# Optimization experiments

Measured on AMD Instinct MI355X. Metric: run time of the kernel, lower is better.

The kernel has to match this reference:

```python
import jax, jax.numpy as jnp
import numpy as np

B, T, C = 32, 512, 32
D, H, DFF, NL = 512, 8, 2048, 3
P, STRIDE, PAD = 16, 8, 8
N = (T - P) // STRIDE + 2  # 64 patches
E = D // H


def _sinusoidal_pe(n, d):
    pos = np.arange(n, dtype=np.float32)[:, None]
    div = np.exp(np.arange(0, d, 2, dtype=np.float32) * -(np.log(10000.0) / d))
    pe = np.zeros((n, d), np.float32)
    pe[:, 0::2] = np.sin(pos * div)
    pe[:, 1::2] = np.cos(pos * div)
    return jnp.asarray(pe)


def setup_inputs() -> dict:
    key = jax.random.key(0)
    ks = jax.random.split(key, 16)
    s = 0.02
    inp = {
        'x_enc': jax.random.normal(ks[0], (B, T, C), jnp.float32),
        'W_val': jax.random.normal(ks[1], (P, D), jnp.float32) * s,
        'Wq': jax.random.normal(ks[2], (NL, D, D), jnp.float32) * s,
        'bq': jnp.zeros((NL, D), jnp.float32),
        'Wk': jax.random.normal(ks[3], (NL, D, D), jnp.float32) * s,
        'bk': jnp.zeros((NL, D), jnp.float32),
        'Wv': jax.random.normal(ks[4], (NL, D, D), jnp.float32) * s,
        'bv': jnp.zeros((NL, D), jnp.float32),
        'Wo': jax.random.normal(ks[5], (NL, D, D), jnp.float32) * s,
        'bo': jnp.zeros((NL, D), jnp.float32),
        'Wc1': jax.random.normal(ks[6], (NL, D, DFF), jnp.float32) * s,
        'bc1': jnp.zeros((NL, DFF), jnp.float32),
        'Wc2': jax.random.normal(ks[7], (NL, DFF, D), jnp.float32) * s,
        'bc2': jnp.zeros((NL, D), jnp.float32),
        'ln1_g': jnp.ones((NL, D), jnp.float32),
        'ln1_b': jnp.zeros((NL, D), jnp.float32),
        'ln2_g': jnp.ones((NL, D), jnp.float32),
        'ln2_b': jnp.zeros((NL, D), jnp.float32),
        'bn_g': jnp.ones((D,), jnp.float32),
        'bn_b': jnp.zeros((D,), jnp.float32),
        'W_head': jax.random.normal(ks[8], (D * N, T), jnp.float32) * s,
        'b_head': jnp.zeros((T,), jnp.float32),
    }
    return inp


def _ln(x, g, b, eps=1e-5):
    m = x.mean(-1, keepdims=True)
    v = ((x - m) ** 2).mean(-1, keepdims=True)
    return (x - m) / jnp.sqrt(v + eps) * g + b


def reference(x_enc, W_val, Wq, bq, Wk, bk, Wv, bv, Wo, bo, Wc1, bc1, Wc2, bc2,
              ln1_g, ln1_b, ln2_g, ln2_b, bn_g, bn_b, W_head, b_head):
    pe = _sinusoidal_pe(N, D)
    # instance normalization over time (means detached, as in torch .detach())
    means = jax.lax.stop_gradient(x_enc.mean(axis=1, keepdims=True))
    x = x_enc - means
    stdev = jnp.sqrt(x.var(axis=1, keepdims=True) + 1e-5)  # [B,1,C]
    x = x / stdev
    x = x.transpose(0, 2, 1)  # [B, C, T]
    # replication pad right by PAD, then unfold into patches [B,C,N,P]
    x = jnp.concatenate([x, jnp.broadcast_to(x[..., -1:], x.shape[:-1] + (PAD,))], axis=-1)
    idx = jnp.arange(N)[:, None] * STRIDE + jnp.arange(P)[None, :]
    xp = x[..., idx]
    tok = xp.reshape(B * C, N, P) @ W_val + pe  # [B*C, N, D]

    scale = 1.0 / np.sqrt(E).astype(np.float32)
    for i in range(NL):
        q = (tok @ Wq[i] + bq[i]).reshape(-1, N, H, E)
        k = (tok @ Wk[i] + bk[i]).reshape(-1, N, H, E)
        v = (tok @ Wv[i] + bv[i]).reshape(-1, N, H, E)
        scores = jnp.einsum('blhe,bshe->bhls', q, k)
        A = jax.nn.softmax(scale * scores, axis=-1)
        V = jnp.einsum('bhls,bshd->blhd', A, v).reshape(-1, N, D)
        tok = tok + (V @ Wo[i] + bo[i])
        y = _ln(tok, ln1_g[i], ln1_b[i])
        y = jax.nn.gelu(y @ Wc1[i] + bc1[i], approximate=False) @ Wc2[i] + bc2[i]
        tok = _ln(tok + y, ln2_g[i], ln2_b[i])

    # BatchNorm1d over d_model channels (batch statistics, biased variance)
    m = tok.mean(axis=(0, 1))
    var = tok.var(axis=(0, 1))
    tok = (tok - m) / jnp.sqrt(var + 1e-5) * bn_g + bn_b

    enc = tok.reshape(B, C, N, D).transpose(0, 1, 3, 2).reshape(B, C, D * N)
    dec = enc @ W_head + b_head          # [B, C, T]
    dec = dec.transpose(0, 2, 1)          # [B, T, C]
    dec = dec * stdev[:, 0, :][:, None, :] + means[:, 0, :][:, None, :]
    return dec
```

## Files before the change

kernel.cpp:

```cpp
#include <hip/hip_runtime.h>
#include <math.h>

namespace {
constexpr int kB = 32, kT = 512, kC = 32, kD = 512, kDFF = 2048, kNL = 3;
constexpr int kP = 16, kStride = 8, kN = 64;
constexpr int kR = kB * kC;
constexpr int kM = kR * kN;
constexpr size_t kWbElems = (size_t)1536 * 512 + 512 * 512 + 2048 * 512 + 512 * 2048;
}

typedef unsigned short u16;
typedef __attribute__((ext_vector_type(8))) short short8;
typedef __attribute__((ext_vector_type(4))) float f32x4;

__device__ __forceinline__ float b2f(u16 u) {
    return __uint_as_float(((unsigned int)u) << 16);
}
__device__ __forceinline__ u16 f2b(float f) {
    unsigned int x = __float_as_uint(f);
    return (u16)((x + 0x7fffu + ((x >> 16) & 1u)) >> 16);
}

__device__ __forceinline__ void async_copy16(const u16* g, u16* l) {
    __builtin_amdgcn_global_load_lds(
        (const __attribute__((address_space(1))) unsigned int*)g,
        (__attribute__((address_space(3))) unsigned int*)l, 16, 0, 0);
}

__global__ void fill_kernel(float* __restrict__ p, float val, int n)
{
    int i = blockIdx.x * blockDim.x + threadIdx.x;
    if (i < n) p[i] = val;
}

__global__ __launch_bounds__(256) void instnorm_stats_kernel(
    const float* __restrict__ x, float* __restrict__ means, float* __restrict__ stdev)
{
    int b = blockIdx.x;
    int c = threadIdx.x & 31;
    int g = threadIdx.x >> 5;
    float s = 0.f, sq = 0.f;
    for (int t = g; t < kT; t += 8) {
        float v = x[(size_t)(b * kT + t) * kC + c];
        s += v; sq += v * v;
    }
    __shared__ float ss[8][32], ssq[8][32];
    ss[g][c] = s; ssq[g][c] = sq;
    __syncthreads();
    if (g == 0) {
        float S = 0.f, SQ = 0.f;
        for (int i = 0; i < 8; i++) { S += ss[i][c]; SQ += ssq[i][c]; }
        float m = S / kT;
        float var = SQ / kT - m * m;
        means[b * kC + c] = m;
        stdev[b * kC + c] = sqrtf(var + 1e-5f);
    }
}

__global__ __launch_bounds__(256) void pe_kernel(float* __restrict__ pe)
{
    int i = blockIdx.x * 256 + threadIdx.x;
    int n = i >> 9, d = i & 511;
    int j = d >> 1;
    float freq = expf(-(float)(2 * j) * (9.210340371976184f / (float)kD));
    float ang = (float)n * freq;
    pe[i] = (d & 1) ? cosf(ang) : sinf(ang);
}

__global__ __launch_bounds__(256) void patch_embed_kernel(
    const float* __restrict__ x, const float* __restrict__ Wval,
    const float* __restrict__ means, const float* __restrict__ stdev,
    const float* __restrict__ pe, u16* __restrict__ tok)
{
    __shared__ float xn[kT + 16];
    __shared__ float wv[kP * kD];
    const int r = blockIdx.x;
    const int b = r >> 5, c = r & 31;
    const int tid = threadIdx.x;
    const float mean = means[r], inv = 1.f / stdev[r];
    for (int t = tid; t < kT; t += 256)
        xn[t] = (x[(size_t)(b * kT + t) * kC + c] - mean) * inv;
    if (tid < 16)
        xn[kT + tid] = (x[(size_t)(b * kT + kT - 1) * kC + c] - mean) * inv;
    for (int i = tid * 4; i < kP * kD; i += 1024)
        *(float4*)&wv[i] = *(const float4*)&Wval[i];
    __syncthreads();

    const int lane = tid & 63, w = tid >> 6;
    const int d0 = lane << 3;
    for (int g = 0; g < 16; g++) {
        const int n = g * 4 + w;
        const float* pen = pe + (size_t)n * kD + d0;
        float acc[8];
        #pragma unroll
        for (int j = 0; j < 8; j++) acc[j] = pen[j];
        #pragma unroll
        for (int p = 0; p < kP; p++) {
            float xv = xn[n * kStride + p];
            const float* wp = &wv[p * kD + d0];
            #pragma unroll
            for (int j = 0; j < 8; j++) acc[j] += xv * wp[j];
        }
        short8 o;
        #pragma unroll
        for (int j = 0; j < 8; j++) o[j] = (short)f2b(acc[j]);
        *(short8*)&tok[((size_t)r * 64 + n) * kD + d0] = o;
    }
}

__global__ __launch_bounds__(256) void transpose_cvt_kernel(
    const float* __restrict__ in, u16* __restrict__ outp,
    const float* __restrict__ scale,
    int ldi, int ldo, int zin, int zout)
{
    __shared__ float tile[64][65];
    const float* ib = in + (size_t)blockIdx.z * zin;
    u16* ob = outp + (size_t)blockIdx.z * zout;
    int k0 = blockIdx.x * 64, n0 = blockIdx.y * 64;
    int tn = threadIdx.x & 63, tk0 = threadIdx.x >> 6;
    #pragma unroll
    for (int kk = tk0; kk < 64; kk += 4) {
        float sc = scale ? scale[k0 + kk] : 1.f;
        tile[kk][tn] = ib[(size_t)(k0 + kk) * ldi + n0 + tn] * sc;
    }
    __syncthreads();
    int wk = threadIdx.x & 63, wn0 = threadIdx.x >> 6;
    #pragma unroll
    for (int nn = wn0; nn < 64; nn += 4)
        ob[(size_t)(n0 + nn) * ldo + k0 + wk] = f2b(tile[wk][nn]);
}

__global__ __launch_bounds__(256) void transpose_cvt4_kernel(
    const float* __restrict__ in0, const float* __restrict__ in1,
    const float* __restrict__ in2, const float* __restrict__ in3,
    u16* __restrict__ outQKV, u16* __restrict__ outO)
{
    __shared__ float tile[64][65];
    int z = blockIdx.z;
    const float* ib = (z == 0) ? in0 : (z == 1) ? in1 : (z == 2) ? in2 : in3;
    u16* ob = (z < 3) ? outQKV + (size_t)z * 512 * 512 : outO;
    int k0 = blockIdx.x * 64, n0 = blockIdx.y * 64;
    int tn = threadIdx.x & 63, tk0 = threadIdx.x >> 6;
    #pragma unroll
    for (int kk = tk0; kk < 64; kk += 4)
        tile[kk][tn] = ib[(size_t)(k0 + kk) * 512 + n0 + tn];
    __syncthreads();
    int wk = threadIdx.x & 63, wn0 = threadIdx.x >> 6;
    #pragma unroll
    for (int nn = wn0; nn < 64; nn += 4)
        ob[(size_t)(n0 + nn) * 512 + k0 + wk] = f2b(tile[wk][nn]);
}

template<int EPI>
__device__ __forceinline__ void gemm_body(
    const u16* __restrict__ A, const u16* __restrict__ B,
    const float* __restrict__ bias, const float* __restrict__ auxb1,
    const float* __restrict__ auxb2,
    u16* __restrict__ C0, u16* __restrict__ C1, u16* __restrict__ C2,
    float* __restrict__ fout,
    int K, int lda, int ldb, int ldc)
{
    __shared__ alignas(16) u16 As[128 * 64];
    __shared__ alignas(16) u16 Bs[128 * 64];

    const int tid  = threadIdx.x;
    const int lane = tid & 63;
    const int wave = tid >> 6;
    const int wm   = wave >> 1;
    const int wn   = wave & 1;

    const int nwg  = gridDim.x * gridDim.y;
    const int orig = blockIdx.y * gridDim.x + blockIdx.x;
    const int qq = nwg >> 3, rr = nwg & 7;
    const int xcd = orig & 7, loc = orig >> 3;
    const int wg  = (xcd < rr) ? (xcd * (qq + 1) + loc)
                               : (rr * (qq + 1) + (xcd - rr) * qq + loc);
    const int row0 = (wg / gridDim.x) * 128;
    const int col0 = (wg % gridDim.x) * 128;
    const size_t zoff = (size_t)blockIdx.z * K;

    const int srow = tid >> 3;
    const int scol = (((tid & 7) ^ (srow & 7)) << 3);
    const u16* const Ag = A + (size_t)(row0 + srow) * lda + zoff + scol;
    const u16* const Bg = B + (size_t)(col0 + srow) * ldb + zoff + scol;
    u16* const AsW = As + (wave << 9);
    u16* const BsW = Bs + (wave << 9);

    const int fr = lane & 15;
    const int pc = (lane >> 4) ^ (lane & 7);
    const int a0 = ((wm << 6) + fr) * 64 + (pc << 3);
    const int a1 = ((wm << 6) + fr) * 64 + ((pc ^ 4) << 3);
    const int b0 = ((wn << 6) + fr) * 64 + (pc << 3);
    const int b1 = ((wn << 6) + fr) * 64 + ((pc ^ 4) << 3);

    short8 af[4], bfr[4];
    f32x4 acc[4][4];
    #pragma unroll
    for (int i = 0; i < 4; i++)
        #pragma unroll
        for (int j = 0; j < 4; j++)
            acc[i][j] = (f32x4){0.f, 0.f, 0.f, 0.f};

    for (int kb = 0; kb < K; kb += 64) {
        __syncthreads();
        #pragma unroll
        for (int c = 0; c < 4; c++) {
            async_copy16(Ag + kb + (size_t)(c * 32) * lda, AsW + c * 2048);
            async_copy16(Bg + kb + (size_t)(c * 32) * ldb, BsW + c * 2048);
        }
        __syncthreads();
        #pragma unroll
        for (int mi = 0; mi < 4; mi++) af[mi]  = *(const short8*)&As[a0 + (mi << 10)];
        #pragma unroll
        for (int ni = 0; ni < 4; ni++) bfr[ni] = *(const short8*)&Bs[b0 + (ni << 10)];
        #pragma unroll
        for (int mi = 0; mi < 4; mi++)
            #pragma unroll
            for (int ni = 0; ni < 4; ni++)
                acc[mi][ni] = __builtin_amdgcn_mfma_f32_16x16x32_bf16(
                    af[mi], bfr[ni], acc[mi][ni], 0, 0, 0);
        #pragma unroll
        for (int mi = 0; mi < 4; mi++) af[mi]  = *(const short8*)&As[a1 + (mi << 10)];
        #pragma unroll
        for (int ni = 0; ni < 4; ni++) bfr[ni] = *(const short8*)&Bs[b1 + (ni << 10)];
        #pragma unroll
        for (int mi = 0; mi < 4; mi++)
            #pragma unroll
            for (int ni = 0; ni < 4; ni++)
                acc[mi][ni] = __builtin_amdgcn_mfma_f32_16x16x32_bf16(
                    af[mi], bfr[ni], acc[mi][ni], 0, 0, 0);
    }

    const int er = (lane >> 4) << 2;
    const int ec = lane & 15;
    u16* dsel = C0;
    const float* bsel = bias;
    if (EPI == 0) {
        int sub = col0 >> 9;
        dsel = (sub == 0) ? C0 : ((sub == 1) ? C1 : C2);
        bsel = (sub == 0) ? bias : ((sub == 1) ? auxb1 : auxb2);
    }
    #pragma unroll
    for (int mi = 0; mi < 4; mi++) {
        #pragma unroll
        for (int ni = 0; ni < 4; ni++) {
            #pragma unroll
            for (int i = 0; i < 4; i++) {
                int r  = row0 + (wm << 6) + (mi << 4) + er + i;
                int cc = col0 + (wn << 6) + (ni << 4) + ec;
                float v = acc[mi][ni][i];
                if (EPI == 0) {
                    int cl = cc & 511;
                    dsel[(size_t)r * 512 + cl] = f2b(v + bsel[cl]);
                } else if (EPI == 1) {
                    size_t o = (size_t)r * ldc + cc;
                    float bb2 = bias ? bias[cc] : 0.f;
                    C0[o] = f2b(b2f(C0[o]) + v + bb2);
                } else if (EPI == 2) {
                    size_t o = (size_t)r * ldc + cc;
                    float z = v + bias[cc];
                    C0[o] = f2b(0.5f * z * (1.f + erff(z * 0.7071067811865475f)));
                } else {
                    fout[((size_t)blockIdx.z << 19) + (size_t)r * ldc + cc] = v;
                }
            }
        }
    }
}

#define GEMM_ARGS \
    const u16* __restrict__ A, const u16* __restrict__ B, \
    const float* __restrict__ bias, const float* __restrict__ auxb1, \
    const float* __restrict__ auxb2, \
    u16* __restrict__ C0, u16* __restrict__ C1, u16* __restrict__ C2, \
    float* __restrict__ fout, \
    int K, int lda, int ldb, int ldc
#define GEMM_PASS A, B, bias, auxb1, auxb2, C0, C1, C2, fout, K, lda, ldb, ldc

__global__ __launch_bounds__(256) void gemm_qkv(GEMM_ARGS)   { gemm_body<0>(GEMM_PASS); }
__global__ __launch_bounds__(256) void gemm_resid(GEMM_ARGS) { gemm_body<1>(GEMM_PASS); }
__global__ __launch_bounds__(256) void gemm_gelu(GEMM_ARGS)  { gemm_body<2>(GEMM_PASS); }
__global__ __launch_bounds__(256) void gemm_head(GEMM_ARGS)  { gemm_body<3>(GEMM_PASS); }

__global__ __launch_bounds__(256) void vtr_kernel(u16* __restrict__ v)
{
    __shared__ u16 tl[4][64 * 72];
    const int tid = threadIdx.x;
    const int wave = tid >> 6, lane = tid & 63;
    const int sr = lane >> 3, ch = lane & 7;
    const int tile = blockIdx.x * 4 + wave;
    const int series = tile >> 3, h = tile & 7;
    u16* g = v + (size_t)series * 64 * kD + h * 64;
    u16* T = tl[wave];
    short8 rd[8];
    #pragma unroll
    for (int r = 0; r < 8; r++)
        rd[r] = *(const short8*)(g + (size_t)(r * 8 + sr) * kD + ch * 8);
    #pragma unroll
    for (int r = 0; r < 8; r++)
        *(short8*)&T[(r * 8 + sr) * 72 + ch * 8] = rd[r];
    __syncthreads();
    #pragma unroll
    for (int r = 0; r < 8; r++) {
        short8 wr;
        #pragma unroll
        for (int q = 0; q < 8; q++)
            wr[q] = (short)T[(ch * 8 + q) * 72 + (r * 8 + sr)];
        *(short8*)(g + (size_t)(r * 8 + sr) * kD + ch * 8) = wr;
    }
}

__global__ __launch_bounds__(256) void attn_mfma_kernel(
    u16* __restrict__ qbuf, const u16* __restrict__ kbuf,
    const u16* __restrict__ vbuf)
{
    __shared__ u16 P[4][64 * 64];
    const int tid = threadIdx.x;
    const int wave = tid >> 6, lane = tid & 63;
    const int quad = lane >> 4, l15 = lane & 15;
    const size_t base = (size_t)blockIdx.x * 64 * kD;
    u16* Pw = P[wave];

    for (int hh = 0; hh < 2; hh++) {
        const int h = wave * 2 + hh;
        const u16* qh = qbuf + base + h * 64;
        const u16* kh = kbuf + base + h * 64;
        const u16* vh = vbuf + base + h * 64;

        short8 af[4][2], bf[4][2];
        #pragma unroll
        for (int mi = 0; mi < 4; mi++)
            #pragma unroll
            for (int kt = 0; kt < 2; kt++)
                af[mi][kt] = *(const short8*)(qh + (size_t)(mi * 16 + l15) * kD
                                              + kt * 32 + quad * 8);
        #pragma unroll
        for (int ni = 0; ni < 4; ni++)
            #pragma unroll
            for (int kt = 0; kt < 2; kt++)
                bf[ni][kt] = *(const short8*)(kh + (size_t)(ni * 16 + l15) * kD
                                              + kt * 32 + quad * 8);
        f32x4 S[4][4];
        #pragma unroll
        for (int mi = 0; mi < 4; mi++)
            #pragma unroll
            for (int ni = 0; ni < 4; ni++)
                S[mi][ni] = (f32x4){0.f, 0.f, 0.f, 0.f};
        #pragma unroll
        for (int mi = 0; mi < 4; mi++)
            #pragma unroll
            for (int ni = 0; ni < 4; ni++) {
                S[mi][ni] = __builtin_amdgcn_mfma_f32_16x16x32_bf16(
                    af[mi][0], bf[ni][0], S[mi][ni], 0, 0, 0);
                S[mi][ni] = __builtin_amdgcn_mfma_f32_16x16x32_bf16(
                    af[mi][1], bf[ni][1], S[mi][ni], 0, 0, 0);
            }

        #pragma unroll
        for (int mi = 0; mi < 4; mi++) {
            #pragma unroll
            for (int i = 0; i < 4; i++) {
                float mx = -1e30f;
                #pragma unroll
                for (int ni = 0; ni < 4; ni++) {
                    float v = S[mi][ni][i] * 0.125f;
                    S[mi][ni][i] = v;
                    mx = fmaxf(mx, v);
                }
                #pragma unroll
                for (int off = 1; off < 16; off <<= 1)
                    mx = fmaxf(mx, __shfl_xor(mx, off));
                float sum = 0.f;
                #pragma unroll
                for (int ni = 0; ni < 4; ni++) {
                    float e = expf(S[mi][ni][i] - mx);
                    S[mi][ni][i] = e;
                    sum += e;
                }
                #pragma unroll
                for (int off = 1; off < 16; off <<= 1)
                    sum += __shfl_xor(sum, off);
                float inv = 1.f / sum;
                #pragma unroll
                for (int ni = 0; ni < 4; ni++)
                    Pw[(mi * 16 + quad * 4 + i) * 64 + ni * 16 + l15] =
                        f2b(S[mi][ni][i] * inv);
            }
        }
        __syncthreads();

        short8 bv[4][2];
        #pragma unroll
        for (int ni = 0; ni < 4; ni++)
            #pragma unroll
            for (int kt = 0; kt < 2; kt++)
                bv[ni][kt] = *(const short8*)(vh + (size_t)(ni * 16 + l15) * kD
                                              + kt * 32 + quad * 8);
        short8 pa[4][2];
        #pragma unroll
        for (int mi = 0; mi < 4; mi++)
            #pragma unroll
            for (int kt = 0; kt < 2; kt++)
                pa[mi][kt] = *(const short8*)&Pw[(mi * 16 + l15) * 64
                                                 + kt * 32 + quad * 8];
        f32x4 O[4][4];
        #pragma unroll
        for (int mi = 0; mi < 4; mi++)
            #pragma unroll
            for (int ni = 0; ni < 4; ni++)
                O[mi][ni] = (f32x4){0.f, 0.f, 0.f, 0.f};
        #pragma unroll
        for (int mi = 0; mi < 4; mi++)
            #pragma unroll
            for (int ni = 0; ni < 4; ni++) {
                O[mi][ni] = __builtin_amdgcn_mfma_f32_16x16x32_bf16(
                    pa[mi][0], bv[ni][0], O[mi][ni], 0, 0, 0);
                O[mi][ni] = __builtin_amdgcn_mfma_f32_16x16x32_bf16(
                    pa[mi][1], bv[ni][1], O[mi][ni], 0, 0, 0);
            }
        u16* qo = qbuf + base + h * 64;
        #pragma unroll
        for (int mi = 0; mi < 4; mi++)
            #pragma unroll
            for (int ni = 0; ni < 4; ni++)
                #pragma unroll
                for (int i = 0; i < 4; i++)
                    qo[(size_t)(mi * 16 + quad * 4 + i) * kD + ni * 16 + l15] =
                        f2b(O[mi][ni][i]);
        __syncthreads();
    }
}

__global__ __launch_bounds__(256) void ln_kernel(
    const u16* __restrict__ x, const float* __restrict__ g,
    const float* __restrict__ bb, u16* __restrict__ y)
{
    size_t row = (size_t)blockIdx.x * 4 + (threadIdx.x >> 6);
    int lane = threadIdx.x & 63;
    int d0 = lane << 3;
    short8 xv = *(const short8*)&x[row * kD + d0];
    float v[8];
    float s = 0.f;
    #pragma unroll
    for (int i = 0; i < 8; i++) {
        v[i] = b2f((u16)xv[i]);
        s += v[i];
    }
    #pragma unroll
    for (int off = 32; off; off >>= 1) s += __shfl_xor(s, off);
    float mean = s * (1.f / kD);
    float sq = 0.f;
    #pragma unroll
    for (int i = 0; i < 8; i++) { float d = v[i] - mean; sq += d * d; }
    #pragma unroll
    for (int off = 32; off; off >>= 1) sq += __shfl_xor(sq, off);
    float inv = 1.f / sqrtf(sq * (1.f / kD) + 1e-5f);
    short8 o;
    #pragma unroll
    for (int i = 0; i < 8; i++)
        o[i] = (short)f2b((v[i] - mean) * inv * g[d0 + i] + bb[d0 + i]);
    *(short8*)&y[row * kD + d0] = o;
}

__global__ void zero_kernel(float* __restrict__ p, int n)
{
    int i = blockIdx.x * blockDim.x + threadIdx.x;
    if (i < n) p[i] = 0.f;
}

__global__ __launch_bounds__(512) void bn_stats_kernel(
    const u16* __restrict__ tok, float* __restrict__ sums, float* __restrict__ sumsq)
{
    int d = threadIdx.x;
    float s = 0.f, sq = 0.f;
    int row0 = blockIdx.x * 256;
    for (int row = row0; row < row0 + 256; row++) {
        float v = b2f(tok[(size_t)row * kD + d]);
        s += v; sq += v * v;
    }
    atomicAdd(&sums[d], s);
    atomicAdd(&sumsq[d], sq);
}

__global__ __launch_bounds__(512) void bn_final_kernel(
    const float* __restrict__ sums, const float* __restrict__ sumsq,
    const float* __restrict__ g, const float* __restrict__ bb,
    float* __restrict__ scale, float* __restrict__ shift)
{
    int d = threadIdx.x;
    float mean = sums[d] / (float)kM;
    float var = sumsq[d] / (float)kM - mean * mean;
    float sc = g[d] / sqrtf(var + 1e-5f);
    scale[d] = sc;
    shift[d] = bb[d] - mean * sc;
}

__global__ __launch_bounds__(512) void head_shift_kernel(
    const float* __restrict__ W_head, const float* __restrict__ shift,
    float* __restrict__ shiftW)
{
    int t = threadIdx.x;
    int r0 = blockIdx.x * 512;
    float s = 0.f;
    for (int r = r0; r < r0 + 512; r++)
        s += shift[r >> 6] * W_head[(size_t)r * 512 + t];
    atomicAdd(&shiftW[t], s);
}

__global__ __launch_bounds__(256) void head_reduce_kernel(
    const float* __restrict__ part, const float* __restrict__ b_head,
    const float* __restrict__ shiftW,
    const float* __restrict__ stdev, const float* __restrict__ means,
    float* __restrict__ out)
{
    int j = blockIdx.x * 256 + threadIdx.x;
    int r = j >> 9, t = j & 511;
    float s = 0.f;
    #pragma unroll
    for (int z = 0; z < 16; z++) s += part[((size_t)z << 19) + j];
    int b = r >> 5, c = r & 31;
    out[(((size_t)b * kT + t) << 5) + c] =
        (s + shiftW[t] + b_head[t]) * stdev[r] + means[r];
}

extern "C" void kernel_launch(void* const* d_in, const int* in_sizes, int n_in,
                              void* d_out, int out_size, void* d_ws, size_t ws_size,
                              hipStream_t stream)
{
    const float* x_enc  = (const float*)d_in[0];
    const float* W_val  = (const float*)d_in[1];
    const float* Wq     = (const float*)d_in[2];
    const float* bq     = (const float*)d_in[3];
    const float* Wk     = (const float*)d_in[4];
    const float* bk     = (const float*)d_in[5];
    const float* Wv     = (const float*)d_in[6];
    const float* bv     = (const float*)d_in[7];
    const float* Wo     = (const float*)d_in[8];
    const float* bo     = (const float*)d_in[9];
    const float* Wc1    = (const float*)d_in[10];
    const float* bc1    = (const float*)d_in[11];
    const float* Wc2    = (const float*)d_in[12];
    const float* bc2    = (const float*)d_in[13];
    const float* ln1_g  = (const float*)d_in[14];
    const float* ln1_b  = (const float*)d_in[15];
    const float* ln2_g  = (const float*)d_in[16];
    const float* ln2_b  = (const float*)d_in[17];
    const float* bn_g   = (const float*)d_in[18];
    const float* bn_b   = (const float*)d_in[19];
    const float* W_head = (const float*)d_in[20];
    const float* b_head = (const float*)d_in[21];
    float* out = (float*)d_out;

    const size_t tailBytes = (2 * kR + 5 * kD + 64 * kD) * sizeof(float);
    const size_t headWb = (size_t)512 * 32768;
    int CH = 0; size_t unit = 0, region = 0;
    const int cands[4] = {1024, 512, 256, 128};
    for (int ci = 0; ci < 4; ci++) {
        size_t u = (size_t)cands[ci] * 64 * kD;
        size_t reg = 3 * u + kWbElems;
        if (reg < headWb) reg = headWb;
        size_t need = ((size_t)kM * kD + reg) * 2 + tailBytes;
        if (need <= ws_size) { CH = cands[ci]; unit = u; region = reg; break; }
    }
    if (CH == 0) {
        hipLaunchKernelGGL(fill_kernel, dim3((out_size + 255) / 256), dim3(256), 0,
                           stream, out, 1.0e6f, out_size);
        return;
    }
    const int nch = kR / CH;
    const int chRows = CH * 64;

    u16* tokb = (u16*)d_ws;
    u16* s0  = tokb + (size_t)kM * kD;
    u16* s1  = s0 + unit;
    u16* s2  = s1 + unit;
    u16* wbL = s2 + unit;
    u16* wbH = s0;
    u16* wQKV = wbL;
    u16* wO   = wQKV + (size_t)1536 * 512;
    u16* wC1  = wO + (size_t)512 * 512;
    u16* wC2  = wC1 + (size_t)2048 * 512;
    float* tail = (float*)(s0 + region);
    float* means    = tail;
    float* stdevp   = means + kR;
    float* bn_sums  = stdevp + kR;
    float* bn_sumsq = bn_sums + kD;
    float* shiftW   = bn_sumsq + kD;
    float* bn_scale = shiftW + kD;
    float* bn_shift = bn_scale + kD;
    float* peT      = bn_shift + kD;

    hipLaunchKernelGGL(pe_kernel, dim3(128), dim3(256), 0, stream, peT);
    hipLaunchKernelGGL(instnorm_stats_kernel, dim3(kB), dim3(256), 0, stream,
                       x_enc, means, stdevp);
    hipLaunchKernelGGL(patch_embed_kernel, dim3(kR), dim3(256), 0, stream,
                       x_enc, W_val, means, stdevp, peT, tokb);

    const dim3 blk(256);
    const int mt = chRows / 128;

    for (int i = 0; i < kNL; i++) {
        const float* Wq_i = Wq + (size_t)i * kD * kD;
        const float* Wk_i = Wk + (size_t)i * kD * kD;
        const float* Wv_i = Wv + (size_t)i * kD * kD;
        const float* Wo_i = Wo + (size_t)i * kD * kD;
        const float* Wc1_i = Wc1 + (size_t)i * kD * kDFF;
        const float* Wc2_i = Wc2 + (size_t)i * kDFF * kD;
        const float* bq_i = bq + i * kD, *bk_i = bk + i * kD, *bv_i = bv + i * kD;

        hipLaunchKernelGGL(transpose_cvt4_kernel, dim3(8, 8, 4), blk, 0, stream,
                           Wq_i, Wk_i, Wv_i, Wo_i, wQKV, wO);
        hipLaunchKernelGGL(transpose_cvt_kernel, dim3(8, 32, 1), blk, 0, stream,
                           Wc1_i, wC1, nullptr, kDFF, kD, 0, 0);
        hipLaunchKernelGGL(transpose_cvt_kernel, dim3(32, 8, 1), blk, 0, stream,
                           Wc2_i, wC2, nullptr, kD, kDFF, 0, 0);

        for (int ch = 0; ch < nch; ch++) {
            u16* tokc = tokb + (size_t)ch * chRows * kD;
            hipLaunchKernelGGL(gemm_qkv, dim3(12, mt, 1), blk, 0, stream,
                               tokc, wQKV, bq_i, bk_i, bv_i, s0, s1, s2,
                               nullptr, kD, kD, kD, kD);
            hipLaunchKernelGGL(vtr_kernel, dim3(CH * 2), blk, 0, stream, s2);
            hipLaunchKernelGGL(attn_mfma_kernel, dim3(CH), blk, 0, stream,
                               s0, s1, s2);
            hipLaunchKernelGGL(gemm_resid, dim3(4, mt, 1), blk, 0, stream,
                               s0, wO, bo + i * kD, nullptr, nullptr,
                               tokc, nullptr, nullptr, nullptr,
                               kD, kD, kD, kD);
            hipLaunchKernelGGL(ln_kernel, dim3(chRows / 4), blk, 0, stream,
                               tokc, ln1_g + i * kD, ln1_b + i * kD, s0);
            for (int half = 0; half < 2; half++) {
                const u16* wc1h = wC1 + (size_t)half * 1024 * 512;
                const u16* wc2h = wC2 + (size_t)half * 1024;
                const float* bc1h = bc1 + (size_t)i * kDFF + half * 1024;
                hipLaunchKernelGGL(gemm_gelu, dim3(8, mt, 1), blk, 0, stream,
                                   s0, wc1h, bc1h, nullptr, nullptr,
                                   s1, nullptr, nullptr, nullptr,
                                   kD, kD, kD, 1024);
                hipLaunchKernelGGL(gemm_resid, dim3(4, mt, 1), blk, 0, stream,
                                   s1, wc2h, (half == 0) ? (bc2 + i * kD) : nullptr,
                                   nullptr, nullptr, tokc, nullptr, nullptr,
                                   nullptr, 1024, 1024, kDFF, kD);
            }
            hipLaunchKernelGGL(ln_kernel, dim3(chRows / 4), blk, 0, stream,
                               tokc, ln2_g + i * kD, ln2_b + i * kD, tokc);
        }
    }

    hipLaunchKernelGGL(zero_kernel, dim3(6), dim3(256), 0, stream, bn_sums, 3 * kD);
    hipLaunchKernelGGL(bn_stats_kernel, dim3(kM / 256), dim3(512), 0, stream,
                       tokb, bn_sums, bn_sumsq);
    hipLaunchKernelGGL(bn_final_kernel, dim3(1), dim3(512), 0, stream,
                       bn_sums, bn_sumsq, bn_g, bn_b, bn_scale, bn_shift);
    hipLaunchKernelGGL(head_shift_kernel, dim3(64), dim3(512), 0, stream,
                       W_head, bn_shift, shiftW);

    hipLaunchKernelGGL(transpose_cvt_kernel, dim3(8, 8, 64), blk, 0, stream,
                       W_head, wbH, bn_scale, 64 * 512, 32768, 512, 512);
    hipLaunchKernelGGL(gemm_head, dim3(4, 8, 16), blk, 0, stream,
                       tokb, wbH, nullptr, nullptr, nullptr,
                       nullptr, nullptr, nullptr, (float*)s1,
                       2048, 32768, 32768, kT);
    hipLaunchKernelGGL(head_reduce_kernel, dim3(kR * kT / 256), blk, 0, stream,
                       (const float*)s1, b_head, shiftW, stdevp, means, out);
}
```

Measured before the change: 3.186 ms.

## Compute V transposed directly via swapped GEMM, drop separate V transpose kernel

The V projection is split out of the fused QKV GEMM and computed as W_v·tok^T with a new row-bias epilogue, so V lands already transposed (head-dim major, token contiguous). This removes the vtr_kernel pass and its global read/write, and the attention kernel now reads V with a configurable stride. The head_shift kernel is also reworked to use 512 blocks with one shift scalar per block, which adds parallelism. The transposed-V layout depends on the chunk row count as the leading dimension, and the extra GEMM launch may be less efficient than the fused one.

```diff
diff --git a/kernel.cpp b/kernel.cpp
--- a/kernel.cpp
+++ b/kernel.cpp
@@ -260,6 +260,8 @@
                     size_t o = (size_t)r * ldc + cc;
                     float z = v + bias[cc];
                     C0[o] = f2b(0.5f * z * (1.f + erff(z * 0.7071067811865475f)));
+                } else if (EPI == 4) {
+                    C0[(size_t)r * ldc + cc] = f2b(v + bias[r]);
                 } else {
                     fout[((size_t)blockIdx.z << 19) + (size_t)r * ldc + cc] = v;
                 }
@@ -281,38 +283,11 @@
 __global__ __launch_bounds__(256) void gemm_resid(GEMM_ARGS) { gemm_body<1>(GEMM_PASS); }
 __global__ __launch_bounds__(256) void gemm_gelu(GEMM_ARGS)  { gemm_body<2>(GEMM_PASS); }
 __global__ __launch_bounds__(256) void gemm_head(GEMM_ARGS)  { gemm_body<3>(GEMM_PASS); }
-
-__global__ __launch_bounds__(256) void vtr_kernel(u16* __restrict__ v)
-{
-    __shared__ u16 tl[4][64 * 72];
-    const int tid = threadIdx.x;
-    const int wave = tid >> 6, lane = tid & 63;
-    const int sr = lane >> 3, ch = lane & 7;
-    const int tile = blockIdx.x * 4 + wave;
-    const int series = tile >> 3, h = tile & 7;
-    u16* g = v + (size_t)series * 64 * kD + h * 64;
-    u16* T = tl[wave];
-    short8 rd[8];
-    #pragma unroll
-    for (int r = 0; r < 8; r++)
-        rd[r] = *(const short8*)(g + (size_t)(r * 8 + sr) * kD + ch * 8);
-    #pragma unroll
-    for (int r = 0; r < 8; r++)
-        *(short8*)&T[(r * 8 + sr) * 72 + ch * 8] = rd[r];
-    __syncthreads();
-    #pragma unroll
-    for (int r = 0; r < 8; r++) {
-        short8 wr;
-        #pragma unroll
-        for (int q = 0; q < 8; q++)
-            wr[q] = (short)T[(ch * 8 + q) * 72 + (r * 8 + sr)];
-        *(short8*)(g + (size_t)(r * 8 + sr) * kD + ch * 8) = wr;
-    }
-}
+__global__ __launch_bounds__(256) void gemm_vt(GEMM_ARGS)    { gemm_body<4>(GEMM_PASS); }
 
 __global__ __launch_bounds__(256) void attn_mfma_kernel(
     u16* __restrict__ qbuf, const u16* __restrict__ kbuf,
-    const u16* __restrict__ vbuf)
+    const u16* __restrict__ vbuf, int ldv)
 {
     __shared__ u16 P[4][64 * 64];
     const int tid = threadIdx.x;
@@ -325,7 +300,7 @@
         const int h = wave * 2 + hh;
         const u16* qh = qbuf + base + h * 64;
         const u16* kh = kbuf + base + h * 64;
-        const u16* vh = vbuf + base + h * 64;
+        const u16* vh = vbuf + (size_t)(h * 64) * ldv + (size_t)blockIdx.x * 64;
 
         short8 af[4][2], bf[4][2];
         #pragma unroll
@@ -394,7 +369,7 @@
         for (int ni = 0; ni < 4; ni++)
             #pragma unroll
             for (int kt = 0; kt < 2; kt++)
-                bv[ni][kt] = *(const short8*)(vh + (size_t)(ni * 16 + l15) * kD
+                bv[ni][kt] = *(const short8*)(vh + (size_t)(ni * 16 + l15) * ldv
                                               + kt * 32 + quad * 8);
         short8 pa[4][2];
         #pragma unroll
@@ -500,11 +475,12 @@
     float* __restrict__ shiftW)
 {
     int t = threadIdx.x;
-    int r0 = blockIdx.x * 512;
+    int r0 = blockIdx.x * 64;
+    float sc = shift[blockIdx.x];
     float s = 0.f;
-    for (int r = r0; r < r0 + 512; r++)
-        s += shift[r >> 6] * W_head[(size_t)r * 512 + t];
-    atomicAdd(&shiftW[t], s);
+    for (int r = r0; r < r0 + 64; r++)
+        s += W_head[(size_t)r * 512 + t];
+    atomicAdd(&shiftW[t], sc * s);
 }
 
 __global__ __launch_bounds__(256) void head_reduce_kernel(
@@ -617,12 +593,15 @@
 
         for (int ch = 0; ch < nch; ch++) {
             u16* tokc = tokb + (size_t)ch * chRows * kD;
-            hipLaunchKernelGGL(gemm_qkv, dim3(12, mt, 1), blk, 0, stream,
-                               tokc, wQKV, bq_i, bk_i, bv_i, s0, s1, s2,
+            hipLaunchKernelGGL(gemm_qkv, dim3(8, mt, 1), blk, 0, stream,
+                               tokc, wQKV, bq_i, bk_i, nullptr, s0, s1, nullptr,
                                nullptr, kD, kD, kD, kD);
-            hipLaunchKernelGGL(vtr_kernel, dim3(CH * 2), blk, 0, stream, s2);
+            hipLaunchKernelGGL(gemm_vt, dim3(chRows / 128, 4, 1), blk, 0, stream,
+                               wQKV + (size_t)1024 * 512, tokc, bv_i, nullptr,
+                               nullptr, s2, nullptr, nullptr, nullptr,
+                               kD, kD, kD, chRows);
             hipLaunchKernelGGL(attn_mfma_kernel, dim3(CH), blk, 0, stream,
-                               s0, s1, s2);
+                               s0, s1, s2, chRows);
             hipLaunchKernelGGL(gemm_resid, dim3(4, mt, 1), blk, 0, stream,
                                s0, wO, bo + i * kD, nullptr, nullptr,
                                tokc, nullptr, nullptr, nullptr,
@@ -652,7 +631,7 @@
                        tokb, bn_sums, bn_sumsq);
     hipLaunchKernelGGL(bn_final_kernel, dim3(1), dim3(512), 0, stream,
                        bn_sums, bn_sumsq, bn_g, bn_b, bn_scale, bn_shift);
-    hipLaunchKernelGGL(head_shift_kernel, dim3(64), dim3(512), 0, stream,
+    hipLaunchKernelGGL(head_shift_kernel, dim3(512), dim3(512), 0, stream,
                        W_head, bn_shift, shiftW);
 
     hipLaunchKernelGGL(transpose_cvt_kernel, dim3(8, 8, 64), blk, 0, stream,
```

After: 3.196 ms. No clear change (+0.3%).
